# Optimization experiments

Measured on AMD Instinct MI355X. Metric: run time of the kernel, lower is better.

The kernel has to match this reference:

```python
import jax, jax.numpy as jnp
import numpy as np
from jax import lax

B, W, S, D, H, BH, C = 32, 128, 192, 768, 10, 30, 50
NEG = -1e30  # stand-in for -inf to keep grads NaN-free


def _lstm_dir(x, Wih, Whh, bih, bhh, reverse):
    # x: [B, T, D] -> [B, T, H]; torch gate order i, f, g, o
    xg = jnp.einsum('btd,gd->btg', x, Wih) + bih  # [B, T, 4H]
    if reverse:
        xg = xg[:, ::-1]

    def step(carry, g_t):
        h, c = carry
        g = g_t + h @ Whh.T + bhh
        i, f, gg, o = jnp.split(g, 4, axis=-1)
        c = jax.nn.sigmoid(f) * c + jax.nn.sigmoid(i) * jnp.tanh(gg)
        h = jax.nn.sigmoid(o) * jnp.tanh(c)
        return (h, c), h

    init = (jnp.zeros((x.shape[0], H), x.dtype), jnp.zeros((x.shape[0], H), x.dtype))
    _, hs = lax.scan(step, init, xg.transpose(1, 0, 2))
    hs = hs.transpose(1, 0, 2)
    if reverse:
        hs = hs[:, ::-1]
    return hs


def _biaffine(x, W1, b1, W2, b2, U, bias):
    # DeepBiaffineScorer: MLP+ReLU on each side, bilinear with bias-augmented inputs
    h1 = jax.nn.relu(x @ W1 + b1)
    h2 = jax.nn.relu(x @ W2 + b2)
    ones = jnp.ones(h1.shape[:-1] + (1,), h1.dtype)
    h1a = jnp.concatenate([h1, ones], -1)  # [B, W, BH+1]
    h2a = jnp.concatenate([h2, ones], -1)
    return jnp.einsum('bih,ohg,bjg->bijo', h1a, U, h2a) + bias  # [B, W, W, O]


def _ce_sum(logits, targets, ignore):
    # cross-entropy, reduction='sum', with ignore_index; classes on last axis
    logp = jax.nn.log_softmax(logits, -1)
    valid = targets != ignore
    t = jnp.where(valid, targets, 0)
    picked = jnp.take_along_axis(logp, t[..., None], -1).squeeze(-1)
    return -jnp.sum(jnp.where(valid, picked, 0.0))


def _forward(hiddens, bert2toks, heads, dep_rels, masks,
             Wih_f, Whh_f, bih_f, bhh_f, Wih_b, Whh_b, bih_b, bhh_b,
             un_W1, un_b1, un_W2, un_b2, un_U, un_bias,
             dr_W1, dr_b1, dr_W2, dr_b2, dr_U, dr_bias):
    # mean of the 3 selected BERT layers, then ragged subtoken -> word mean pooling
    means = jnp.mean(hiddens, axis=0)  # [B, S+1, D]
    sub = means[:, 1:]                 # skip [CLS]: [B, S, D]
    seg_sum = jax.vmap(lambda x, s: jax.ops.segment_sum(x, s, num_segments=W))(sub, bert2toks)
    cnt = jax.vmap(lambda s: jax.ops.segment_sum(jnp.ones((S,), sub.dtype), s, num_segments=W))(bert2toks)
    bert_out = seg_sum / jnp.maximum(cnt, 1.0)[..., None]  # [B, W, D]

    # BiLSTM (sent_lens are all full length W, so packing is the identity)
    fwd = _lstm_dir(bert_out, Wih_f, Whh_f, bih_f, bhh_f, False)
    bwd = _lstm_dir(bert_out, Wih_b, Whh_b, bih_b, bhh_b, True)
    unpacked = jnp.concatenate([fwd, bwd], -1)  # [B, W, 2H]

    unlabeled = _biaffine(unpacked, un_W1, un_b1, un_W2, un_b2, un_U, un_bias)[..., 0]  # [B, W, W]
    deprel = _biaffine(unpacked, dr_W1, dr_b1, dr_W2, dr_b2, dr_U, dr_bias)             # [B, W, W, C]

    eye = jnp.eye(W, dtype=bool)
    unlabeled = jnp.where(eye[None], NEG, unlabeled)

    # gather gold-head deprel scores: [B, W, C]
    head_scores = jnp.take_along_axis(deprel, heads[:, :, None, None], axis=2).squeeze(2)
    heads_ = jnp.where(masks, -1, heads)

    deprel_loss = _ce_sum(head_scores, dep_rels, 0)
    depind_loss = _ce_sum(unlabeled[:, 1:], heads_[:, 1:], -1)
    return deprel_loss + depind_loss


def setup_inputs() -> dict:
    key = jax.random.key(0)
    ks = jax.random.split(key, 26)
    hiddens = jax.random.normal(ks[0], (3, B, S + 1, D), jnp.float32)
    # non-decreasing subtoken->word map covering all W words
    bert2toks = jnp.broadcast_to((jnp.arange(S) * W) // S, (B, S)).astype(jnp.int32)
    heads = jax.random.randint(ks[1], (B, W), 0, W)
    heads = jnp.where(heads == jnp.arange(W)[None, :], 0, heads)  # no self-head (diag is -inf)
    dep_rels = jax.random.randint(ks[2], (B, W), 0, C)
    masks = jnp.zeros((B, W), bool)
    sent_lens = jnp.full((B,), W, jnp.int32)
    s = 0.1
    p = lambda k, shape: jax.random.normal(k, shape, jnp.float32) * s
    return dict(
        hiddens=hiddens, bert2toks=bert2toks, heads=heads, dep_rels=dep_rels,
        masks=masks, sent_lens=sent_lens,
        Wih_f=p(ks[3], (4 * H, D)), Whh_f=p(ks[4], (4 * H, H)), bih_f=p(ks[5], (4 * H,)), bhh_f=p(ks[6], (4 * H,)),
        Wih_b=p(ks[7], (4 * H, D)), Whh_b=p(ks[8], (4 * H, H)), bih_b=p(ks[9], (4 * H,)), bhh_b=p(ks[10], (4 * H,)),
        un_W1=p(ks[11], (2 * H, BH)), un_b1=p(ks[12], (BH,)), un_W2=p(ks[13], (2 * H, BH)), un_b2=p(ks[14], (BH,)),
        un_U=p(ks[15], (1, BH + 1, BH + 1)), un_bias=p(ks[16], (1,)),
        dr_W1=p(ks[17], (2 * H, BH)), dr_b1=p(ks[18], (BH,)), dr_W2=p(ks[19], (2 * H, BH)), dr_b2=p(ks[20], (BH,)),
        dr_U=p(ks[21], (C, BH + 1, BH + 1)), dr_bias=p(ks[22], (C,)),
    )


def reference(hiddens, bert2toks, heads, dep_rels, masks, sent_lens,
              Wih_f, Whh_f, bih_f, bhh_f, Wih_b, Whh_b, bih_b, bhh_b,
              un_W1, un_b1, un_W2, un_b2, un_U, un_bias,
              dr_W1, dr_b1, dr_W2, dr_b2, dr_U, dr_bias):
    # sent_lens unused: all sentences are full length, so pack/unpack is identity
    return _forward(hiddens, bert2toks, heads, dep_rels, masks,
                    Wih_f, Whh_f, bih_f, bhh_f, Wih_b, Whh_b, bih_b, bhh_b,
                    un_W1, un_b1, un_W2, un_b2, un_U, un_bias,
                    dr_W1, dr_b1, dr_W2, dr_b2, dr_U, dr_bias)
```

## Files before the change

kernel.cpp:

```cpp
#include <hip/hip_runtime.h>

#define Bn 32
#define Wn 128
#define Sn 192
#define Dn 768
#define Hn 10
#define BHn 30
#define Cn 50
#define CAP 8
#define NEGV -1e30f

__device__ __forceinline__ float fsig(float x) {
    return __builtin_amdgcn_rcpf(1.0f + __expf(-x));
}
__device__ __forceinline__ float ftanh(float x) {
    return 1.0f - 2.0f * __builtin_amdgcn_rcpf(1.0f + __expf(2.0f * x));
}
__device__ __forceinline__ float lane_bcast(float v, int srclane) {
    union { float f; int i; } u, w;
    u.f = v;
    w.i = __builtin_amdgcn_readlane(u.i, srclane);
    return w.f;
}
template <int Q>
__device__ __forceinline__ float quad_bcast(float v) {
    union { float f; int i; } u, w;
    u.f = v;
    w.i = __builtin_amdgcn_mov_dpp(u.i, (Q << 6) | (Q << 4) | (Q << 2) | Q, 0xf, 0xf, true);
    return w.f;
}

__global__ void k_zero(int* cnt, float* out) {
    int i = blockIdx.x * blockDim.x + threadIdx.x;
    if (i < Bn * Wn) cnt[i] = 0;
    if (i == 0) out[0] = 0.f;
}

__global__ void k_lists(const int* __restrict__ b2t, int* cnt, int* lists) {
    int idx = blockIdx.x * blockDim.x + threadIdx.x;
    if (idx >= Bn * Sn) return;
    int b = idx / Sn;
    int w = b2t[idx];
    if (w < 0 || w >= Wn) return;
    int s = idx % Sn;
    int pos = atomicAdd(&cnt[b * Wn + w], 1);
    if (pos < CAP) lists[(b * Wn + w) * CAP + pos] = s;
}

#define XSTR 196
#define WSTR 68
__global__ __launch_bounds__(256) void k_tokproj(const float* __restrict__ hid,
                                                 const float* __restrict__ Wf,
                                                 const float* __restrict__ Wb,
                                                 float* __restrict__ tokg4) {
    __shared__ float xl[64 * XSTR];
    __shared__ float wl[80 * WSTR];
    int tb = blockIdx.x >> 2;
    int kq = blockIdx.x & 3;
    int b = tb / 3;
    int s0 = (tb % 3) * 64;
    int k0 = kq * 192;
    int tid = threadIdx.x;

    for (int idx = tid; idx < 64 * 48; idx += 256) {
        int r = idx / 48, k4 = idx % 48;
        size_t rowbase = ((size_t)b * (Sn + 1) + (s0 + r + 1)) * Dn + k0 + 4 * k4;
        float4 v0 = *(const float4*)(hid + rowbase);
        float4 v1 = *(const float4*)(hid + (size_t)Bn * (Sn + 1) * Dn + rowbase);
        float4 v2 = *(const float4*)(hid + (size_t)2 * Bn * (Sn + 1) * Dn + rowbase);
        float4 v;
        v.x = v0.x + v1.x + v2.x; v.y = v0.y + v1.y + v2.y;
        v.z = v0.z + v1.z + v2.z; v.w = v0.w + v1.w + v2.w;
        *(float4*)(xl + r * XSTR + 4 * k4) = v;
    }

    int tg = tid >> 4;
    int rg = tid & 15;
    float acc[4][5];
#pragma unroll
    for (int tt = 0; tt < 4; ++tt)
#pragma unroll
        for (int rr = 0; rr < 5; ++rr) acc[tt][rr] = 0.f;

    for (int c = 0; c < 3; ++c) {
        __syncthreads();
        for (int idx = tid; idx < 80 * 16; idx += 256) {
            int co = idx >> 4, k4c = idx & 15;
            int dir = co / 40, off = co % 40;
            int j = off >> 2, g = off & 3;
            const float* src = (dir ? Wb : Wf) + (g * 10 + j) * Dn + k0 + c * 64 + 4 * k4c;
            *(float4*)(wl + co * WSTR + 4 * k4c) = *(const float4*)src;
        }
        __syncthreads();
#pragma unroll 2
        for (int k4c = 0; k4c < 16; ++k4c) {
            float4 xv[4], wv[5];
#pragma unroll
            for (int tt = 0; tt < 4; ++tt)
                xv[tt] = *(const float4*)(xl + (tg * 4 + tt) * XSTR + c * 64 + 4 * k4c);
#pragma unroll
            for (int rr = 0; rr < 5; ++rr)
                wv[rr] = *(const float4*)(wl + (rg * 5 + rr) * WSTR + 4 * k4c);
#pragma unroll
            for (int tt = 0; tt < 4; ++tt)
#pragma unroll
                for (int rr = 0; rr < 5; ++rr) {
                    acc[tt][rr] += xv[tt].x * wv[rr].x + xv[tt].y * wv[rr].y
                                 + xv[tt].z * wv[rr].z + xv[tt].w * wv[rr].w;
                }
        }
    }
    size_t nbase = (size_t)kq * (Bn * Sn) + (size_t)b * Sn + s0;
#pragma unroll
    for (int tt = 0; tt < 4; ++tt) {
        size_t ob = (nbase + tg * 4 + tt) * 80 + rg * 5;
#pragma unroll
        for (int rr = 0; rr < 5; ++rr) tokg4[ob + rr] = acc[tt][rr];
    }
}

__global__ __launch_bounds__(128) void k_wordmean(const float* __restrict__ tokg4,
                                                  const int* __restrict__ cnt,
                                                  const int* __restrict__ lists,
                                                  const float* __restrict__ bih_f,
                                                  const float* __restrict__ bih_b,
                                                  float* __restrict__ xg) {
    const size_t NT80 = (size_t)Bn * Sn * 80;
    int bw = blockIdx.x;
    int b = bw / Wn, w = bw % Wn;
    int l = threadIdx.x;
    if (l >= 80) return;
    int dir = l / 40, off = l % 40;
    int c = cnt[bw];
    int cc = c < CAP ? c : CAP;
    float acc = 0.f;
    for (int tk = 0; tk < cc; ++tk) {
        int s = lists[bw * CAP + tk];
        size_t base = ((size_t)b * Sn + s) * 80 + l;
        acc += tokg4[base] + tokg4[base + NT80]
             + tokg4[base + 2 * NT80] + tokg4[base + 3 * NT80];
    }
    float inv = 1.0f / (3.0f * (float)(c > 0 ? c : 1));
    int brow = (off & 3) * 10 + (off >> 2);
    float bias = (dir ? bih_b : bih_f)[brow];
    xg[((size_t)(dir * Bn + b) * Wn + w) * 40 + off] = acc * inv + bias;
}

__global__ __launch_bounds__(64) void k_lstm(const float* __restrict__ xg,
                                             const float* __restrict__ Whh_f, const float* __restrict__ bhh_f,
                                             const float* __restrict__ Whh_b, const float* __restrict__ bhh_b,
                                             float* __restrict__ hs) {
    int lane = threadIdx.x;
    int seq = blockIdx.x;
    int dir = seq >> 5;
    int l = lane < 40 ? lane : 39;
    int j = l >> 2, G = l & 3;

    const float* Whh = dir ? Whh_b : Whh_f;
    const float* bhh = dir ? bhh_b : bhh_f;
    float wk[Hn];
#pragma unroll
    for (int k = 0; k < Hn; ++k) wk[k] = Whh[(G * Hn + j) * Hn + k];
    float bias = bhh[G * Hn + j];

    const float* xbase = xg + (size_t)seq * Wn * 40;
    float* hbase = hs + (size_t)seq * Wn * Hn;
    bool st = (G == 0) && (lane < 40);

    float h = 0.f, c = 0.f;
    int dt = dir ? -1 : 1;
    int t = dir ? (Wn - 1) : 0;
    float xq[4];
    xq[0] = xbase[t * 40 + l];
    xq[1] = xbase[(t + dt) * 40 + l];
    xq[2] = xbase[(t + 2 * dt) * 40 + l];

#pragma unroll 4
    for (int step = 0; step < Wn; ++step) {
        float xv = xq[step & 3];
        xq[(step + 3) & 3] = xbase[(t + 3 * dt) * 40 + l];
        float hb[Hn];
#pragma unroll
        for (int k = 0; k < Hn; ++k) hb[k] = lane_bcast(h, 4 * k);
        float ga = xv, gb = bias;
#pragma unroll
        for (int k = 0; k < 5; ++k) ga += wk[k] * hb[k];
#pragma unroll
        for (int k = 5; k < Hn; ++k) gb += wk[k] * hb[k];
        float g = ga + gb;
        float gin = (G == 2) ? 2.f * g : g;
        float s = fsig(gin);
        float av = (G == 2) ? 2.f * s - 1.f : s;
        float ai = quad_bcast<0>(av);
        float af = quad_bcast<1>(av);
        float ag = quad_bcast<2>(av);
        float ao = quad_bcast<3>(av);
        c = af * c + ai * ag;
        h = ao * ftanh(c);
        if (st) hbase[t * Hn + j] = h;
        t += dt;
    }
}

__global__ __launch_bounds__(128) void k_mlp(const float* __restrict__ hs,
                                             const float* __restrict__ uW1, const float* __restrict__ ub1,
                                             const float* __restrict__ uW2, const float* __restrict__ ub2,
                                             const float* __restrict__ dW1, const float* __restrict__ db1,
                                             const float* __restrict__ dW2, const float* __restrict__ db2,
                                             float* __restrict__ hpad) {
    int bt = blockIdx.x;
    int b = bt / Wn, t = bt % Wn;
    __shared__ float x[20];
    int tid = threadIdx.x;
    if (tid < 20) {
        x[tid] = (tid < Hn) ? hs[((size_t)(0 * Bn + b) * Wn + t) * Hn + tid]
                            : hs[((size_t)(1 * Bn + b) * Wn + t) * Hn + (tid - Hn)];
    }
    __syncthreads();
    if (tid >= 124) {
        hpad[((size_t)(tid - 124) * Bn * Wn + bt) * 32 + 31] = 0.f;
        return;
    }
    int which = tid / 31, k = tid % 31;
    float v;
    if (k == 30) {
        v = 1.0f;
    } else {
        const float* Wm;
        const float* bv;
        if (which == 0) { Wm = uW1; bv = ub1; }
        else if (which == 1) { Wm = uW2; bv = ub2; }
        else if (which == 2) { Wm = dW1; bv = db1; }
        else { Wm = dW2; bv = db2; }
        float a = bv[k];
#pragma unroll
        for (int d = 0; d < 20; ++d) a += x[d] * Wm[d * BHn + k];
        v = a > 0.f ? a : 0.f;
    }
    hpad[((size_t)which * Bn * Wn + bt) * 32 + k] = v;
}

__global__ __launch_bounds__(256) void k_gather(const float* __restrict__ hpad,
                                                const int* __restrict__ heads,
                                                float* __restrict__ h2g) {
    int idx = blockIdx.x * 256 + threadIdx.x;
    int n = idx >> 3, q = idx & 7;
    int b = n >> 7;
    int jh = heads[n];
    if (jh < 0 || jh >= Wn) jh = 0;
    const float4* src = (const float4*)(hpad + ((size_t)3 * Bn * Wn + b * Wn + jh) * 32);
    ((float4*)(h2g + (size_t)n * 32))[q] = src[q];
}

__global__ __launch_bounds__(256) void k_drscore(const float* __restrict__ h1g,
                                                 const float* __restrict__ h2g,
                                                 const float* __restrict__ U, const float* __restrict__ dbias,
                                                 float* __restrict__ sc) {
    int nc = blockIdx.x & 63;
    int oq = blockIdx.x >> 6;
    __shared__ float Ul[4][992];
    int tid = threadIdx.x;
    for (int idx = tid; idx < 4 * 992; idx += 256) {
        int o = idx / 992, r = idx - o * 992;
        int h = r >> 5, g = r & 31;
        int oo = oq * 4 + o; if (oo >= Cn) oo = Cn - 1;
        Ul[o][r] = (g < 31) ? U[(size_t)oo * 961 + h * 31 + g] : 0.f;
    }
    int w = tid >> 6, lane = tid & 63;
    int o = oq * 4 + w;
    int n = nc * 64 + lane;
    float h2r[32];
    {
        const float4* p = (const float4*)(h2g + (size_t)n * 32);
#pragma unroll
        for (int q = 0; q < 8; ++q) {
            float4 v = p[q];
            h2r[4 * q + 0] = v.x; h2r[4 * q + 1] = v.y;
            h2r[4 * q + 2] = v.z; h2r[4 * q + 3] = v.w;
        }
    }
    float h1r[32];
    {
        const float4* p = (const float4*)(h1g + (size_t)n * 32);
#pragma unroll
        for (int q = 0; q < 8; ++q) {
            float4 v = p[q];
            h1r[4 * q + 0] = v.x; h1r[4 * q + 1] = v.y;
            h1r[4 * q + 2] = v.z; h1r[4 * q + 3] = v.w;
        }
    }
    __syncthreads();
    const float* up = Ul[w];
    float acc = 0.f;
    for (int h = 0; h < 31; ++h) {
        float t = 0.f;
#pragma unroll
        for (int g = 0; g < 32; ++g) t += up[h * 32 + g] * h2r[g];
        acc += h1r[h] * t;
    }
    if (o < Cn) sc[(size_t)n * Cn + o] = acc + dbias[o];
}

__global__ __launch_bounds__(256) void k_loss2(const float* __restrict__ hpad,
                                               const float* __restrict__ U0, const float* __restrict__ ubias,
                                               const float* __restrict__ sc,
                                               const int* __restrict__ heads,
                                               const unsigned char* __restrict__ masks,
                                               const int* __restrict__ dep_rels,
                                               float* __restrict__ out) {
    int b = blockIdx.x;
    int tid = threadIdx.x;
    __shared__ float h2s[128 * 36];
    __shared__ float tg[128 * 36];
    __shared__ float U0l[992];
    __shared__ float red[256];
    const float* h1a = hpad + (size_t)b * Wn * 32;
    const float* h2a = hpad + ((size_t)Bn * Wn + b * Wn) * 32;
    for (int idx = tid; idx < 128 * 32; idx += 256)
        h2s[(idx >> 5) * 36 + (idx & 31)] = h2a[idx];
    for (int idx = tid; idx < 992; idx += 256) {
        int g = idx & 31;
        U0l[idx] = (g < 31) ? U0[(idx >> 5) * 31 + g] : 0.f;
    }
    __syncthreads();
    {
        int l = tid & 31, ig = tid >> 5;
        float ur[31];
#pragma unroll
        for (int h = 0; h < 31; ++h) ur[h] = U0l[h * 32 + l];
        for (int ii = 0; ii < 16; ++ii) {
            int i = ig * 16 + ii;
            const float4* hp = (const float4*)(h1a + (size_t)i * 32);
            float hr[32];
#pragma unroll
            for (int q = 0; q < 8; ++q) {
                float4 v = hp[q];
                hr[4 * q] = v.x; hr[4 * q + 1] = v.y; hr[4 * q + 2] = v.z; hr[4 * q + 3] = v.w;
            }
            float a = 0.f;
#pragma unroll
            for (int h = 0; h < 31; ++h) a += hr[h] * ur[h];
            tg[i * 36 + l] = a;
        }
    }
    __syncthreads();
    float acc = 0.f;
    {
        int jg = tid & 7, ig2 = tid >> 3;
        float ub = ubias[0];
        float4 tq[4][8];
#pragma unroll
        for (int ii = 0; ii < 4; ++ii) {
            const float4* tp = (const float4*)(tg + (ig2 * 4 + ii) * 36);
#pragma unroll
            for (int q = 0; q < 8; ++q) tq[ii][q] = tp[q];
        }
        float m[4], lsum[4], sh[4];
        int hd[4];
#pragma unroll
        for (int ii = 0; ii < 4; ++ii) {
            m[ii] = -3e38f; lsum[ii] = 0.f; sh[ii] = 0.f;
            hd[ii] = heads[b * Wn + ig2 * 4 + ii];
        }
        for (int jj = 0; jj < 16; ++jj) {
            int j = jg * 16 + jj;
            const float4* h2p = (const float4*)(h2s + j * 36);
            float4 hq[8];
#pragma unroll
            for (int q = 0; q < 8; ++q) hq[q] = h2p[q];
#pragma unroll
            for (int ii = 0; ii < 4; ++ii) {
                int i = ig2 * 4 + ii;
                float s = ub;
#pragma unroll
                for (int q = 0; q < 8; ++q) {
                    s += tq[ii][q].x * hq[q].x + tq[ii][q].y * hq[q].y
                       + tq[ii][q].z * hq[q].z + tq[ii][q].w * hq[q].w;
                }
                if (j == i) s = NEGV;
                float mn = fmaxf(m[ii], s);
                lsum[ii] = lsum[ii] * __expf(m[ii] - mn) + __expf(s - mn);
                m[ii] = mn;
                if (j == hd[ii]) sh[ii] = s;
            }
        }
#pragma unroll
        for (int ii = 0; ii < 4; ++ii) {
            float shv = (jg == (hd[ii] >> 4)) ? sh[ii] : 0.f;
            float mm = m[ii], ll = lsum[ii];
#pragma unroll
            for (int off = 1; off < 8; off <<= 1) {
                float m2 = __shfl_xor(mm, off);
                float l2 = __shfl_xor(ll, off);
                float mn = fmaxf(mm, m2);
                ll = ll * __expf(mm - mn) + l2 * __expf(m2 - mn);
                mm = mn;
                shv += __shfl_xor(shv, off);
            }
            if (jg == 0) {
                int i = ig2 * 4 + ii;
                if (i >= 1 && !masks[b * Wn + i])
                    acc += -(shv - (mm + __logf(ll)));
            }
        }
    }
    if (tid < 128) {
        int n = b * Wn + tid;
        int r = dep_rels[n];
        if (r != 0 && r < Cn) {
            const float* sp = sc + (size_t)n * Cn;
            float mm = sp[0];
            for (int o = 1; o < Cn; ++o) mm = fmaxf(mm, sp[o]);
            float e = 0.f;
            for (int o = 0; o < Cn; ++o) e += __expf(sp[o] - mm);
            acc += -(sp[r] - (mm + __logf(e)));
        }
    }
    red[tid] = acc;
    __syncthreads();
    for (int off = 128; off > 0; off >>= 1) {
        if (tid < off) red[tid] += red[tid + off];
        __syncthreads();
    }
    if (tid == 0) atomicAdd(out, red[0]);
}

extern "C" void kernel_launch(void* const* d_in, const int* in_sizes, int n_in,
                              void* d_out, int out_size, void* d_ws, size_t ws_size,
                              hipStream_t stream) {
    const float* hiddens = (const float*)d_in[0];
    const int* b2t = (const int*)d_in[1];
    const int* heads = (const int*)d_in[2];
    const int* dep_rels = (const int*)d_in[3];
    const unsigned char* masks = (const unsigned char*)d_in[4];
    const float* Wih_f = (const float*)d_in[6];
    const float* Whh_f = (const float*)d_in[7];
    const float* bih_f = (const float*)d_in[8];
    const float* bhh_f = (const float*)d_in[9];
    const float* Wih_b = (const float*)d_in[10];
    const float* Whh_b = (const float*)d_in[11];
    const float* bih_b = (const float*)d_in[12];
    const float* bhh_b = (const float*)d_in[13];
    const float* un_W1 = (const float*)d_in[14];
    const float* un_b1 = (const float*)d_in[15];
    const float* un_W2 = (const float*)d_in[16];
    const float* un_b2 = (const float*)d_in[17];
    const float* un_U  = (const float*)d_in[18];
    const float* un_bias = (const float*)d_in[19];
    const float* dr_W1 = (const float*)d_in[20];
    const float* dr_b1 = (const float*)d_in[21];
    const float* dr_W2 = (const float*)d_in[22];
    const float* dr_b2 = (const float*)d_in[23];
    const float* dr_U  = (const float*)d_in[24];
    const float* dr_bias = (const float*)d_in[25];

    char* p = (char*)d_ws;
    int* cnt = (int*)p;           p += (size_t)Bn * Wn * 4;
    int* lists = (int*)p;         p += (size_t)Bn * Wn * CAP * 4;
    float* tokg4 = (float*)p;     p += (size_t)4 * Bn * Sn * 80 * 4;
    float* xg = (float*)p;        p += (size_t)2 * Bn * Wn * 40 * 4;
    float* hs = (float*)p;        p += (size_t)2 * Bn * Wn * Hn * 4;
    float* hpad = (float*)p;      p += (size_t)4 * Bn * Wn * 32 * 4;
    float* h2g = (float*)p;       p += (size_t)Bn * Wn * 32 * 4;
    float* sc = (float*)p;        p += (size_t)Bn * Wn * Cn * 4;

    float* out = (float*)d_out;

    k_zero<<<(Bn * Wn + 255) / 256, 256, 0, stream>>>(cnt, out);
    k_lists<<<(Bn * Sn + 255) / 256, 256, 0, stream>>>(b2t, cnt, lists);
    k_tokproj<<<96 * 4, 256, 0, stream>>>(hiddens, Wih_f, Wih_b, tokg4);
    k_wordmean<<<Bn * Wn, 128, 0, stream>>>(tokg4, cnt, lists, bih_f, bih_b, xg);
    k_lstm<<<64, 64, 0, stream>>>(xg, Whh_f, bhh_f, Whh_b, bhh_b, hs);
    k_mlp<<<Bn * Wn, 128, 0, stream>>>(hs, un_W1, un_b1, un_W2, un_b2,
                                       dr_W1, dr_b1, dr_W2, dr_b2, hpad);
    k_gather<<<Bn * Wn * 8 / 256, 256, 0, stream>>>(hpad, heads, h2g);
    k_drscore<<<13 * 64, 256, 0, stream>>>(hpad + (size_t)2 * Bn * Wn * 32, h2g, dr_U, dr_bias, sc);
    k_loss2<<<Bn, 256, 0, stream>>>(hpad, un_U, un_bias, sc, heads, masks, dep_rels, out);
}
```

Baseline: 116.3 us.

## Split token projection over eight K-chunks and loss kernel over row quarters

The token projection kernel now splits the 768-wide reduction into eight 96-wide chunks instead of four, which doubles the block count and shrinks shared memory per block. In exchange it writes twice as many partial sums, and the word-mean kernel must read eight partials per token. The biaffine loss kernel is split into four blocks per sentence, each handling 32 rows with one row per 8-thread group, and the j loop start is staggered per thread to spread shared-memory bank accesses. This raises parallelism on a 32-block kernel, at the cost of each block reloading h2 and U0 and more atomic adds.

```diff
diff --git a/kernel.cpp b/kernel.cpp
--- a/kernel.cpp
+++ b/kernel.cpp
@@ -47,23 +47,23 @@
     if (pos < CAP) lists[(b * Wn + w) * CAP + pos] = s;
 }
 
-#define XSTR 196
-#define WSTR 68
+#define XSTR 100
+#define WSTR 52
 __global__ __launch_bounds__(256) void k_tokproj(const float* __restrict__ hid,
                                                  const float* __restrict__ Wf,
                                                  const float* __restrict__ Wb,
                                                  float* __restrict__ tokg4) {
     __shared__ float xl[64 * XSTR];
     __shared__ float wl[80 * WSTR];
-    int tb = blockIdx.x >> 2;
-    int kq = blockIdx.x & 3;
+    int tb = blockIdx.x >> 3;
+    int kq = blockIdx.x & 7;
     int b = tb / 3;
     int s0 = (tb % 3) * 64;
-    int k0 = kq * 192;
+    int k0 = kq * 96;
     int tid = threadIdx.x;
 
-    for (int idx = tid; idx < 64 * 48; idx += 256) {
-        int r = idx / 48, k4 = idx % 48;
+    for (int idx = tid; idx < 64 * 24; idx += 256) {
+        int r = idx / 24, k4 = idx % 24;
         size_t rowbase = ((size_t)b * (Sn + 1) + (s0 + r + 1)) * Dn + k0 + 4 * k4;
         float4 v0 = *(const float4*)(hid + rowbase);
         float4 v1 = *(const float4*)(hid + (size_t)Bn * (Sn + 1) * Dn + rowbase);
@@ -82,22 +82,22 @@
 #pragma unroll
         for (int rr = 0; rr < 5; ++rr) acc[tt][rr] = 0.f;
 
-    for (int c = 0; c < 3; ++c) {
+    for (int c = 0; c < 2; ++c) {
         __syncthreads();
-        for (int idx = tid; idx < 80 * 16; idx += 256) {
-            int co = idx >> 4, k4c = idx & 15;
+        for (int idx = tid; idx < 80 * 12; idx += 256) {
+            int co = idx / 12, k4c = idx % 12;
             int dir = co / 40, off = co % 40;
             int j = off >> 2, g = off & 3;
-            const float* src = (dir ? Wb : Wf) + (g * 10 + j) * Dn + k0 + c * 64 + 4 * k4c;
+            const float* src = (dir ? Wb : Wf) + (g * 10 + j) * Dn + k0 + c * 48 + 4 * k4c;
             *(float4*)(wl + co * WSTR + 4 * k4c) = *(const float4*)src;
         }
         __syncthreads();
 #pragma unroll 2
-        for (int k4c = 0; k4c < 16; ++k4c) {
+        for (int k4c = 0; k4c < 12; ++k4c) {
             float4 xv[4], wv[5];
 #pragma unroll
             for (int tt = 0; tt < 4; ++tt)
-                xv[tt] = *(const float4*)(xl + (tg * 4 + tt) * XSTR + c * 64 + 4 * k4c);
+                xv[tt] = *(const float4*)(xl + (tg * 4 + tt) * XSTR + c * 48 + 4 * k4c);
 #pragma unroll
             for (int rr = 0; rr < 5; ++rr)
                 wv[rr] = *(const float4*)(wl + (rg * 5 + rr) * WSTR + 4 * k4c);
@@ -137,8 +137,8 @@
     for (int tk = 0; tk < cc; ++tk) {
         int s = lists[bw * CAP + tk];
         size_t base = ((size_t)b * Sn + s) * 80 + l;
-        acc += tokg4[base] + tokg4[base + NT80]
-             + tokg4[base + 2 * NT80] + tokg4[base + 3 * NT80];
+#pragma unroll
+        for (int p = 0; p < 8; ++p) acc += tokg4[base + p * NT80];
     }
     float inv = 1.0f / (3.0f * (float)(c > 0 ? c : 1));
     int brow = (off & 3) * 10 + (off >> 2);
@@ -308,10 +308,11 @@
                                                const unsigned char* __restrict__ masks,
                                                const int* __restrict__ dep_rels,
                                                float* __restrict__ out) {
-    int b = blockIdx.x;
+    int b = blockIdx.x >> 2;
+    int ic = blockIdx.x & 3;
     int tid = threadIdx.x;
     __shared__ float h2s[128 * 36];
-    __shared__ float tg[128 * 36];
+    __shared__ float tg[32 * 36];
     __shared__ float U0l[992];
     __shared__ float red[256];
     const float* h1a = hpad + (size_t)b * Wn * 32;
@@ -328,8 +329,9 @@
         float ur[31];
 #pragma unroll
         for (int h = 0; h < 31; ++h) ur[h] = U0l[h * 32 + l];
-        for (int ii = 0; ii < 16; ++ii) {
-            int i = ig * 16 + ii;
+        for (int ii = 0; ii < 4; ++ii) {
+            int il = ig * 4 + ii;
+            int i = ic * 32 + il;
             const float4* hp = (const float4*)(h1a + (size_t)i * 32);
             float hr[32];
 #pragma unroll
@@ -340,72 +342,52 @@
             float a = 0.f;
 #pragma unroll
             for (int h = 0; h < 31; ++h) a += hr[h] * ur[h];
-            tg[i * 36 + l] = a;
+            tg[il * 36 + l] = a;
         }
     }
     __syncthreads();
     float acc = 0.f;
     {
-        int jg = tid & 7, ig2 = tid >> 3;
+        int jg = tid & 7, il = tid >> 3;
+        int i = ic * 32 + il;
         float ub = ubias[0];
-        float4 tq[4][8];
-#pragma unroll
-        for (int ii = 0; ii < 4; ++ii) {
-            const float4* tp = (const float4*)(tg + (ig2 * 4 + ii) * 36);
-#pragma unroll
-            for (int q = 0; q < 8; ++q) tq[ii][q] = tp[q];
-        }
-        float m[4], lsum[4], sh[4];
-        int hd[4];
-#pragma unroll
-        for (int ii = 0; ii < 4; ++ii) {
-            m[ii] = -3e38f; lsum[ii] = 0.f; sh[ii] = 0.f;
-            hd[ii] = heads[b * Wn + ig2 * 4 + ii];
-        }
+        float4 tq[8];
+        const float4* tp = (const float4*)(tg + il * 36);
+#pragma unroll
+        for (int q = 0; q < 8; ++q) tq[q] = tp[q];
+        float m = -3e38f, lsum = 0.f, sh = 0.f;
+        int hd = heads[b * Wn + i];
         for (int jj = 0; jj < 16; ++jj) {
-            int j = jg * 16 + jj;
+            int j = jg * 16 + ((jj + jg) & 15);
             const float4* h2p = (const float4*)(h2s + j * 36);
-            float4 hq[8];
-#pragma unroll
-            for (int q = 0; q < 8; ++q) hq[q] = h2p[q];
-#pragma unroll
-            for (int ii = 0; ii < 4; ++ii) {
-                int i = ig2 * 4 + ii;
-                float s = ub;
-#pragma unroll
-                for (int q = 0; q < 8; ++q) {
-                    s += tq[ii][q].x * hq[q].x + tq[ii][q].y * hq[q].y
-                       + tq[ii][q].z * hq[q].z + tq[ii][q].w * hq[q].w;
-                }
-                if (j == i) s = NEGV;
-                float mn = fmaxf(m[ii], s);
-                lsum[ii] = lsum[ii] * __expf(m[ii] - mn) + __expf(s - mn);
-                m[ii] = mn;
-                if (j == hd[ii]) sh[ii] = s;
+            float s = ub;
+#pragma unroll
+            for (int q = 0; q < 8; ++q) {
+                float4 hq = h2p[q];
+                s += tq[q].x * hq.x + tq[q].y * hq.y + tq[q].z * hq.z + tq[q].w * hq.w;
             }
-        }
-#pragma unroll
-        for (int ii = 0; ii < 4; ++ii) {
-            float shv = (jg == (hd[ii] >> 4)) ? sh[ii] : 0.f;
-            float mm = m[ii], ll = lsum[ii];
-#pragma unroll
-            for (int off = 1; off < 8; off <<= 1) {
-                float m2 = __shfl_xor(mm, off);
-                float l2 = __shfl_xor(ll, off);
-                float mn = fmaxf(mm, m2);
-                ll = ll * __expf(mm - mn) + l2 * __expf(m2 - mn);
-                mm = mn;
-                shv += __shfl_xor(shv, off);
-            }
-            if (jg == 0) {
-                int i = ig2 * 4 + ii;
-                if (i >= 1 && !masks[b * Wn + i])
-                    acc += -(shv - (mm + __logf(ll)));
-            }
-        }
-    }
-    if (tid < 128) {
-        int n = b * Wn + tid;
+            if (j == i) s = NEGV;
+            float mn = fmaxf(m, s);
+            lsum = lsum * __expf(m - mn) + __expf(s - mn);
+            m = mn;
+            if (j == hd) sh = s;
+        }
+        float shv = (jg == (hd >> 4)) ? sh : 0.f;
+        float mm = m, ll = lsum;
+#pragma unroll
+        for (int off = 1; off < 8; off <<= 1) {
+            float m2 = __shfl_xor(mm, off);
+            float l2 = __shfl_xor(ll, off);
+            float mn = fmaxf(mm, m2);
+            ll = ll * __expf(mm - mn) + l2 * __expf(m2 - mn);
+            mm = mn;
+            shv += __shfl_xor(shv, off);
+        }
+        if (jg == 0 && i >= 1 && !masks[b * Wn + i])
+            acc += -(shv - (mm + __logf(ll)));
+    }
+    if (tid < 32) {
+        int n = b * Wn + ic * 32 + tid;
         int r = dep_rels[n];
         if (r != 0 && r < Cn) {
             const float* sp = sc + (size_t)n * Cn;
@@ -457,7 +439,7 @@
     char* p = (char*)d_ws;
     int* cnt = (int*)p;           p += (size_t)Bn * Wn * 4;
     int* lists = (int*)p;         p += (size_t)Bn * Wn * CAP * 4;
-    float* tokg4 = (float*)p;     p += (size_t)4 * Bn * Sn * 80 * 4;
+    float* tokg4 = (float*)p;     p += (size_t)8 * Bn * Sn * 80 * 4;
     float* xg = (float*)p;        p += (size_t)2 * Bn * Wn * 40 * 4;
     float* hs = (float*)p;        p += (size_t)2 * Bn * Wn * Hn * 4;
     float* hpad = (float*)p;      p += (size_t)4 * Bn * Wn * 32 * 4;
@@ -468,12 +450,12 @@
 
     k_zero<<<(Bn * Wn + 255) / 256, 256, 0, stream>>>(cnt, out);
     k_lists<<<(Bn * Sn + 255) / 256, 256, 0, stream>>>(b2t, cnt, lists);
-    k_tokproj<<<96 * 4, 256, 0, stream>>>(hiddens, Wih_f, Wih_b, tokg4);
+    k_tokproj<<<96 * 8, 256, 0, stream>>>(hiddens, Wih_f, Wih_b, tokg4);
     k_wordmean<<<Bn * Wn, 128, 0, stream>>>(tokg4, cnt, lists, bih_f, bih_b, xg);
     k_lstm<<<64, 64, 0, stream>>>(xg, Whh_f, bhh_f, Whh_b, bhh_b, hs);
     k_mlp<<<Bn * Wn, 128, 0, stream>>>(hs, un_W1, un_b1, un_W2, un_b2,
                                        dr_W1, dr_b1, dr_W2, dr_b2, hpad);
     k_gather<<<Bn * Wn * 8 / 256, 256, 0, stream>>>(hpad, heads, h2g);
     k_drscore<<<13 * 64, 256, 0, stream>>>(hpad + (size_t)2 * Bn * Wn * 32, h2g, dr_U, dr_bias, sc);
-    k_loss2<<<Bn, 256, 0, stream>>>(hpad, un_U, un_bias, sc, heads, masks, dep_rels, out);
-}
+    k_loss2<<<Bn * 4, 256, 0, stream>>>(hpad, un_U, un_bias, sc, heads, masks, dep_rels, out);
+}
```

Result: faster. 100.9 us (-13.3%).
